# Optimization experiments

Hardware: AMD Instinct MI355X
Metric: run time of the kernel (lower is better)

Reference implementation:

```python
import jax, jax.numpy as jnp
import numpy as np

B, S, H, NH = 4, 1024, 2048, 16
HD = H // NH  # 128


def _rotate_half(x):
    x1, x2 = jnp.split(x, 2, axis=-1)
    return jnp.concatenate([-x2, x1], axis=-1)


def setup_inputs() -> dict:
    key = jax.random.key(0)
    ks = jax.random.split(key, 8)
    hidden_states = jax.random.normal(ks[0], (B, S, H), dtype=jnp.float32)
    k_in = jax.random.normal(ks[1], (B * NH, HD, S), dtype=jnp.float32)  # [B*nh, hd, K]
    v_in = jax.random.normal(ks[2], (B, NH, S, HD), dtype=jnp.float32)   # [B, nh, K, hd]
    # causal additive mask [B, 1, Q, K]
    i = jnp.arange(S)[:, None]
    j = jnp.arange(S)[None, :]
    mask = jnp.where(j <= i, 0.0, -1e9).astype(jnp.float32)
    attention_mask = jnp.broadcast_to(mask, (B, 1, S, S))
    # RoPE tables [S, hd]
    inv_freq = 1.0 / (10000.0 ** (jnp.arange(0, HD, 2, dtype=jnp.float32) / HD))
    freqs = jnp.arange(S, dtype=jnp.float32)[:, None] * inv_freq[None, :]  # [S, hd/2]
    emb = jnp.concatenate([freqs, freqs], axis=-1)  # [S, hd]
    rope_cos = jnp.cos(emb)
    rope_sin = jnp.sin(emb)
    std = 0.02
    wq = jax.random.normal(ks[3], (H, H), dtype=jnp.float32) * std
    bq = jnp.zeros((H,), dtype=jnp.float32)
    wo = jax.random.normal(ks[4], (H, H), dtype=jnp.float32) * (std / np.sqrt(2 * 24))
    bo = jnp.zeros((H,), dtype=jnp.float32)
    return {"hidden_states": hidden_states, "key": k_in, "value": v_in,
            "attention_mask": attention_mask, "rope_cos": rope_cos,
            "rope_sin": rope_sin, "wq": wq, "bq": bq, "wo": wo, "bo": bo}


def reference(hidden_states, key, value, attention_mask, rope_cos, rope_sin, wq, bq, wo, bo):
    dtype = hidden_states.dtype
    scale = 1.0 / np.sqrt(HD)
    # q projection -> [B, nh, Q, hd]
    q = hidden_states @ wq.T + bq
    q = q.reshape(B, S, NH, HD).transpose(0, 2, 1, 3)
    # RoPE on query only
    cos = rope_cos[None, None, :, :]
    sin = rope_sin[None, None, :, :]
    q = q * cos + _rotate_half(q) * sin
    # scores: key is [B*nh, hd, K]
    k = key.reshape(B, NH, HD, S)
    scores = jnp.einsum('bhqd,bhdk->bhqk', q, k) * scale + attention_mask
    probs = jax.nn.softmax(scores.astype(jnp.float32), axis=-1).astype(dtype)
    # attention output -> [B, Q, H]
    out = jnp.einsum('bhqk,bhkd->bqhd', probs, value).reshape(B, S, H)
    out = out @ wo.T + bo
    return out
```

## Files before the change

kernel.cpp:

```cpp
#include <hip/hip_runtime.h>
#include <cstdint>


typedef unsigned short u16;
typedef __bf16 bf16x8 __attribute__((ext_vector_type(8)));
typedef float  f32x4  __attribute__((ext_vector_type(4)));
typedef float  f32x16 __attribute__((ext_vector_type(16)));
typedef uint32_t u32x4 __attribute__((ext_vector_type(4)));

__device__ __forceinline__ u16 f2bf(float f) {
  uint32_t u = __builtin_bit_cast(uint32_t, f);
  u += 0x7fffu + ((u >> 16) & 1u);
  return (u16)(u >> 16);
}
__device__ __forceinline__ float bf2f(u16 h) {
  uint32_t u = ((uint32_t)h) << 16;
  return __builtin_bit_cast(float, u);
}
__device__ __forceinline__ uint32_t cvtpk(float lo, float hi) {
  uint32_t r;
  asm("v_cvt_pk_bf16_f32 %0, %1, %2" : "=v"(r) : "v"(lo), "v"(hi));
  return r;
}
__device__ __forceinline__ void gld16(const void* g, void* l) {
  __builtin_amdgcn_global_load_lds(
      (const __attribute__((address_space(1))) void*)g,
      (__attribute__((address_space(3))) void*)l, 16, 0, 0);
}

__global__ __launch_bounds__(256) void cvt_kernel(const float* __restrict__ in,
                                                  u16* __restrict__ out, int n4) {
  int i = blockIdx.x * 256 + threadIdx.x;
  if (i < n4) {
    float4 v = ((const float4*)in)[i];
    ushort4 o;
    o.x = f2bf(v.x); o.y = f2bf(v.y); o.z = f2bf(v.z); o.w = f2bf(v.w);
    ((ushort4*)out)[i] = o;
  }
}

__global__ __launch_bounds__(256) void transpose_cvt(const float* __restrict__ in,
                                                     u16* __restrict__ out, int R, int C) {
  __shared__ float tile[32][33];
  const int bh = blockIdx.x;
  const int nct = C >> 5;
  const int rt = blockIdx.y / nct, ct = blockIdx.y % nct;
  const float* src = in + (size_t)bh * R * C;
  u16* dst = out + (size_t)bh * R * C;
  const int r = threadIdx.x >> 3, c4 = (threadIdx.x & 7) * 4;
  float4 v = *(const float4*)(src + (size_t)(rt * 32 + r) * C + ct * 32 + c4);
  tile[r][c4 + 0] = v.x; tile[r][c4 + 1] = v.y;
  tile[r][c4 + 2] = v.z; tile[r][c4 + 3] = v.w;
  __syncthreads();
  ushort4 o;
  o.x = f2bf(tile[c4 + 0][r]); o.y = f2bf(tile[c4 + 1][r]);
  o.z = f2bf(tile[c4 + 2][r]); o.w = f2bf(tile[c4 + 3][r]);
  *(ushort4*)(dst + (size_t)(ct * 32 + r) * R + rt * 32 + c4) = o;
}

template<bool OUT_BF16>
__global__ __launch_bounds__(256, 2)
void gemm_bt(const u16* __restrict__ A, const u16* __restrict__ Bm,
             const float* __restrict__ bias, void* __restrict__ Cout,
             int M, int N, int K) {
  __shared__ __align__(16) u16 As[128 * 32];
  __shared__ __align__(16) u16 Bs[128 * 32];
  const int t = threadIdx.x, lane = t & 63, w = t >> 6;
  const int row0 = blockIdx.x * 128, col0 = blockIdx.y * 128;
  const int wr = (w >> 1) * 64, wc = (w & 1) * 64;
  const int fr = lane & 15, fg = lane >> 4, fk = fg * 8;
  const int srow = w * 32 + (lane >> 2), scol = (lane & 3) * 8;
  const u16* gA0 = A  + (size_t)(row0 + srow) * K + scol;
  const u16* gB0 = Bm + (size_t)(col0 + srow) * K + scol;
  u16* lA0 = As + (w * 32) * 32;
  u16* lA1 = As + (w * 32 + 16) * 32;
  u16* lB0 = Bs + (w * 32) * 32;
  u16* lB1 = Bs + (w * 32 + 16) * 32;
  f32x4 acc[4][4] = {};

  for (int k0 = 0; k0 < K; k0 += 32) {
    __syncthreads();
    gld16(gA0 + k0, lA0);
    gld16(gA0 + k0 + (size_t)16 * K, lA1);
    gld16(gB0 + k0, lB0);
    gld16(gB0 + k0 + (size_t)16 * K, lB1);
    __syncthreads();
    bf16x8 af[4], bq[4];
#pragma unroll
    for (int i = 0; i < 4; i++) af[i] = *(const bf16x8*)&As[(wr + i * 16 + fr) * 32 + fk];
#pragma unroll
    for (int i = 0; i < 4; i++) bq[i] = *(const bf16x8*)&Bs[(wc + i * 16 + fr) * 32 + fk];
#pragma unroll
    for (int mi = 0; mi < 4; mi++)
#pragma unroll
      for (int ni = 0; ni < 4; ni++)
        acc[mi][ni] = __builtin_amdgcn_mfma_f32_16x16x32_bf16(af[mi], bq[ni], acc[mi][ni], 0, 0, 0);
  }

#pragma unroll
  for (int mi = 0; mi < 4; mi++)
#pragma unroll
    for (int ni = 0; ni < 4; ni++) {
      int col = col0 + wc + ni * 16 + fr;
      float bv = bias[col];
#pragma unroll
      for (int i = 0; i < 4; i++) {
        int row = row0 + wr + mi * 16 + fg * 4 + i;
        float v = acc[mi][ni][i] + bv;
        if constexpr (OUT_BF16) ((u16*)Cout)[(size_t)row * N + col] = f2bf(v);
        else                    ((float*)Cout)[(size_t)row * N + col] = v;
      }
    }
}

__global__ __launch_bounds__(256, 2)
void gemm_rope(const u16* __restrict__ A, const u16* __restrict__ Bm,
               const float* __restrict__ bias, const float* __restrict__ cosb,
               const float* __restrict__ sinb, u16* __restrict__ qout) {
  __shared__ __align__(16) u16 As[128 * 32];
  __shared__ __align__(16) u16 Bs[128 * 32];
  const int K = 2048;
  const float SL2E = 0.12751743f;
  const int t = threadIdx.x, lane = t & 63, w = t >> 6;
  const int row0 = blockIdx.x * 128, h = blockIdx.y;
  const int wr = (w >> 1) * 64, g = w & 1;
  const int fr = lane & 15, fg = lane >> 4, fk = fg * 8;
  const int srow = w * 32 + (lane >> 2), scol = (lane & 3) * 8;
  const u16* gA0 = A  + (size_t)(row0 + srow) * K + scol;
  const u16* gB0 = Bm + (size_t)(h * 128 + srow) * K + scol;
  u16* lA0 = As + (w * 32) * 32;
  u16* lA1 = As + (w * 32 + 16) * 32;
  u16* lB0 = Bs + (w * 32) * 32;
  u16* lB1 = Bs + (w * 32 + 16) * 32;
  f32x4 acc[4][4] = {};
  const int colr[4] = {g * 32 + fr, g * 32 + 16 + fr,
                       g * 32 + 64 + fr, g * 32 + 80 + fr};

  for (int k0 = 0; k0 < K; k0 += 32) {
    __syncthreads();
    gld16(gA0 + k0, lA0);
    gld16(gA0 + k0 + (size_t)16 * K, lA1);
    gld16(gB0 + k0, lB0);
    gld16(gB0 + k0 + (size_t)16 * K, lB1);
    __syncthreads();
    bf16x8 af[4], bq[4];
#pragma unroll
    for (int i = 0; i < 4; i++) af[i] = *(const bf16x8*)&As[(wr + i * 16 + fr) * 32 + fk];
#pragma unroll
    for (int ni = 0; ni < 4; ni++) bq[ni] = *(const bf16x8*)&Bs[colr[ni] * 32 + fk];
#pragma unroll
    for (int mi = 0; mi < 4; mi++)
#pragma unroll
      for (int ni = 0; ni < 4; ni++)
        acc[mi][ni] = __builtin_amdgcn_mfma_f32_16x16x32_bf16(af[mi], bq[ni], acc[mi][ni], 0, 0, 0);
  }

  float bv[4];
#pragma unroll
  for (int ni = 0; ni < 4; ni++) bv[ni] = bias[h * 128 + colr[ni]];
#pragma unroll
  for (int mi = 0; mi < 4; mi++)
#pragma unroll
    for (int i = 0; i < 4; i++) {
      int row = row0 + wr + mi * 16 + fg * 4 + i;
      int s = row & 1023, bb = row >> 10;
      size_t obase = (((size_t)(bb * 16 + h)) * 1024 + s) * 128;
#pragma unroll
      for (int dp = 0; dp < 2; dp++) {
        int d = g * 32 + dp * 16 + fr;
        float c  = cosb[s * 128 + d] * SL2E;
        float sn = sinb[s * 128 + d] * SL2E;
        float qlo = acc[mi][dp][i] + bv[dp];
        float qhi = acc[mi][dp + 2][i] + bv[dp + 2];
        qout[obase + d]      = f2bf(qlo * c - qhi * sn);
        qout[obase + d + 64] = f2bf(qhi * c + qlo * sn);
      }
    }
}

__global__ __launch_bounds__(256, 1)
void attn_kernel(const u16* __restrict__ qbf, const u16* __restrict__ kTb,
                 const u16* __restrict__ vTb, u16* __restrict__ aout) {
  __shared__ __align__(16) u16 Kb[2][64 * 128];
  __shared__ __align__(16) u16 Vb[2][128 * 64];
  const int t = threadIdx.x, lane = t & 63, w = t >> 6;
  const int x = blockIdx.x;
  const int qt = 7 - (x >> 6);
  const int bh = x & 63;
  const int b = bh >> 4, h = bh & 15;
  const int q31 = lane & 31, hi = lane >> 5, kx7 = q31 & 7;
  const u16* kbase = kTb + (size_t)bh * 131072;
  const u16* vbase = vTb + (size_t)bh * 131072;

  const int kRow = t >> 4;
  const int kCb  = (t & 15) ^ (kRow & 7);
  const int vRow = t >> 3;
  const int vCb  = (t & 7) ^ (vRow & 7);

  const int rw0 = qt * 128 + w * 32;
  const int rowg = rw0 + q31;
  const int last = 2 * qt + 1;
  const int wlast = 2 * qt + (w >> 1);

  bf16x8 qf[8];
#pragma unroll
  for (int ds = 0; ds < 8; ds++)
    qf[ds] = *(const bf16x8*)&qbf[((size_t)bh * 1024 + rowg) * 128 + ds * 16 + hi * 8];

  f32x16 acc[4] = {};
  float m = -3e38f, l = 0.f;

  auto STAGE = [&](int kt, int buf) {
    const u16* ks = kbase + (size_t)(kt * 64 + kRow) * 128 + kCb * 8;
    const u16* vs = vbase + (size_t)vRow * 1024 + kt * 64 + vCb * 8;
    u16* kl = &Kb[buf][t * 8];
    u16* vl = &Vb[buf][t * 8];
#pragma unroll
    for (int p = 0; p < 4; p++) {
      gld16(ks + (size_t)p * 16 * 128, kl + p * 2048);
      gld16(vs + (size_t)p * 32 * 1024, vl + p * 2048);
    }
  };

  STAGE(0, 0);
  __syncthreads();
  for (int kt = 0; kt <= last; kt++) {
    const int cur = kt & 1;
    if (kt < last) STAGE(kt + 1, cur ^ 1);
    if (kt <= wlast) {
      f32x16 sa0 = {}, sa1 = {};
      __builtin_amdgcn_s_setprio(1);
#pragma unroll
      for (int ds = 0; ds < 8; ds++) {
        bf16x8 k0 = *(const bf16x8*)&Kb[cur][q31 * 128 + (((2 * ds + hi) ^ kx7) * 8)];
        bf16x8 k1 = *(const bf16x8*)&Kb[cur][(q31 + 32) * 128 + (((2 * ds + hi) ^ kx7) * 8)];
        sa0 = __builtin_amdgcn_mfma_f32_32x32x16_bf16(k0, qf[ds], sa0, 0, 0, 0);
        sa1 = __builtin_amdgcn_mfma_f32_32x32x16_bf16(k1, qf[ds], sa1, 0, 0, 0);
      }
      __builtin_amdgcn_s_setprio(0);

      if (kt == wlast) {
#pragma unroll
        for (int rr = 0; rr < 16; rr++) {
          int cr = (rr & 3) + 8 * (rr >> 2) + 4 * hi;
          if (kt * 64 + cr > rowg)      sa0[rr] = -1e9f;
          if (kt * 64 + 32 + cr > rowg) sa1[rr] = -1e9f;
        }
      }
      float t0 = fmaxf(fmaxf(sa0[0], sa0[1]), sa0[2]);
      float t1 = fmaxf(fmaxf(sa0[3], sa0[4]), sa0[5]);
      float t2 = fmaxf(fmaxf(sa0[6], sa0[7]), sa0[8]);
      float t3 = fmaxf(fmaxf(sa0[9], sa0[10]), sa0[11]);
      float t4 = fmaxf(fmaxf(sa0[12], sa0[13]), sa0[14]);
      float u0 = fmaxf(fmaxf(sa1[0], sa1[1]), sa1[2]);
      float u1 = fmaxf(fmaxf(sa1[3], sa1[4]), sa1[5]);
      float u2 = fmaxf(fmaxf(sa1[6], sa1[7]), sa1[8]);
      float u3 = fmaxf(fmaxf(sa1[9], sa1[10]), sa1[11]);
      float u4 = fmaxf(fmaxf(sa1[12], sa1[13]), sa1[14]);
      float mx = fmaxf(fmaxf(fmaxf(fmaxf(t0, t1), fmaxf(t2, t3)),
                             fmaxf(fmaxf(t4, sa0[15]), fmaxf(u0, u1))),
                       fmaxf(fmaxf(u2, u3), fmaxf(u4, sa1[15])));
      mx = fmaxf(mx, __shfl_xor(mx, 32));
      if (!__all(mx - m <= 11.5f)) {
        float mn = fmaxf(m, mx);
        float corr = __builtin_amdgcn_exp2f(m - mn);
        m = mn; l *= corr;
#pragma unroll
        for (int nd = 0; nd < 4; nd++)
#pragma unroll
          for (int rr = 0; rr < 16; rr++) acc[nd][rr] *= corr;
      }
#pragma unroll
      for (int rr = 0; rr < 16; rr++) {
        sa0[rr] = __builtin_amdgcn_exp2f(sa0[rr] - m);
        sa1[rr] = __builtin_amdgcn_exp2f(sa1[rr] - m);
      }
      {
        float s0 = (sa0[0] + sa0[1]) + (sa0[2] + sa0[3]);
        float s1 = (sa0[4] + sa0[5]) + (sa0[6] + sa0[7]);
        float s2 = (sa0[8] + sa0[9]) + (sa0[10] + sa0[11]);
        float s3 = (sa0[12] + sa0[13]) + (sa0[14] + sa0[15]);
        float s4 = (sa1[0] + sa1[1]) + (sa1[2] + sa1[3]);
        float s5 = (sa1[4] + sa1[5]) + (sa1[6] + sa1[7]);
        float s6 = (sa1[8] + sa1[9]) + (sa1[10] + sa1[11]);
        float s7 = (sa1[12] + sa1[13]) + (sa1[14] + sa1[15]);
        float sum = ((s0 + s1) + (s2 + s3)) + ((s4 + s5) + (s6 + s7));
        sum += __shfl_xor(sum, 32);
        l += sum;
      }

      __builtin_amdgcn_s_setprio(1);
      uint32_t wA = cvtpk(sa0[0], sa0[1]),   wB = cvtpk(sa0[2], sa0[3]);
      uint32_t wC = cvtpk(sa0[4], sa0[5]),   wD = cvtpk(sa0[6], sa0[7]);
      uint32_t wE = cvtpk(sa0[8], sa0[9]),   wF = cvtpk(sa0[10], sa0[11]);
      uint32_t wG = cvtpk(sa0[12], sa0[13]), wH = cvtpk(sa0[14], sa0[15]);
      uint32_t wI = cvtpk(sa1[0], sa1[1]),   wJ = cvtpk(sa1[2], sa1[3]);
      uint32_t wK = cvtpk(sa1[4], sa1[5]),   wL = cvtpk(sa1[6], sa1[7]);
      uint32_t wM = cvtpk(sa1[8], sa1[9]),   wN = cvtpk(sa1[10], sa1[11]);
      uint32_t wO = cvtpk(sa1[12], sa1[13]), wP = cvtpk(sa1[14], sa1[15]);
      uint32_t xA = __shfl_xor(wA, 32), xB = __shfl_xor(wB, 32);
      uint32_t xC = __shfl_xor(wC, 32), xD = __shfl_xor(wD, 32);
      uint32_t xE = __shfl_xor(wE, 32), xF = __shfl_xor(wF, 32);
      uint32_t xG = __shfl_xor(wG, 32), xH = __shfl_xor(wH, 32);
      uint32_t xI = __shfl_xor(wI, 32), xJ = __shfl_xor(wJ, 32);
      uint32_t xK = __shfl_xor(wK, 32), xL = __shfl_xor(wL, 32);
      uint32_t xM = __shfl_xor(wM, 32), xN = __shfl_xor(wN, 32);
      uint32_t xO = __shfl_xor(wO, 32), xP = __shfl_xor(wP, 32);
#pragma unroll
      for (int ks = 0; ks < 4; ks++) {
        u32x4 aw;
        if (ks == 0) {
          aw.x = hi ? xC : wA;  aw.y = hi ? xD : wB;
          aw.z = hi ? wC : xA;  aw.w = hi ? wD : xB;
        } else if (ks == 1) {
          aw.x = hi ? xG : wE;  aw.y = hi ? xH : wF;
          aw.z = hi ? wG : xE;  aw.w = hi ? wH : xF;
        } else if (ks == 2) {
          aw.x = hi ? xK : wI;  aw.y = hi ? xL : wJ;
          aw.z = hi ? wK : xI;  aw.w = hi ? wL : xJ;
        } else {
          aw.x = hi ? xO : wM;  aw.y = hi ? xP : wN;
          aw.z = hi ? wO : xM;  aw.w = hi ? wP : xN;
        }
        bf16x8 af = __builtin_bit_cast(bf16x8, aw);
#pragma unroll
        for (int nd = 0; nd < 4; nd++) {
          bf16x8 vf = *(const bf16x8*)&Vb[cur][(nd * 32 + q31) * 64 + (((2 * ks + hi) ^ kx7) * 8)];
          acc[nd] = __builtin_amdgcn_mfma_f32_32x32x16_bf16(af, vf, acc[nd], 0, 0, 0);
        }
      }
      __builtin_amdgcn_s_setprio(0);
    }
    __syncthreads();
  }

  float linv = 1.f / l;
#pragma unroll
  for (int rr = 0; rr < 16; rr++) {
    int cr = (rr & 3) + 8 * (rr >> 2) + 4 * hi;
    float li = __shfl(linv, cr);
    int sg = rw0 + cr;
    size_t obase = (((size_t)b * 1024 + sg) * 16 + h) * 128 + q31;
#pragma unroll
    for (int nd = 0; nd < 4; nd++)
      aout[obase + nd * 32] = f2bf(acc[nd][rr] * li);
  }
}

extern "C" void kernel_launch(void* const* d_in, const int* in_sizes, int n_in,
                              void* d_out, int out_size, void* d_ws, size_t ws_size,
                              hipStream_t stream) {
  const float* hs  = (const float*)d_in[0];
  const float* key = (const float*)d_in[1];
  const float* val = (const float*)d_in[2];
  const float* rc  = (const float*)d_in[4];
  const float* rs  = (const float*)d_in[5];
  const float* wq  = (const float*)d_in[6];
  const float* bq  = (const float*)d_in[7];
  const float* wo  = (const float*)d_in[8];
  const float* bo  = (const float*)d_in[9];
  float* out = (float*)d_out;

  char* ws = (char*)d_ws;
  u16* hs_bf = (u16*)(ws);
  u16* wq_bf = (u16*)(ws + 16777216);
  u16* wo_bf = (u16*)(ws + 25165824);
  u16* q_bf  = (u16*)(ws + 33554432);
  u16* kT    = (u16*)(ws + 50331648);
  u16* vT    = (u16*)(ws + 67108864);
  u16* attn_bf = hs_bf;

  cvt_kernel<<<8192, 256, 0, stream>>>(hs, hs_bf, 8388608 / 4);
  cvt_kernel<<<4096, 256, 0, stream>>>(wq, wq_bf, 4194304 / 4);
  cvt_kernel<<<4096, 256, 0, stream>>>(wo, wo_bf, 4194304 / 4);

  transpose_cvt<<<dim3(64, 128), 256, 0, stream>>>(key, kT, 128, 1024);
  transpose_cvt<<<dim3(64, 128), 256, 0, stream>>>(val, vT, 1024, 128);

  gemm_rope<<<dim3(32, 16), 256, 0, stream>>>(hs_bf, wq_bf, bq, rc, rs, q_bf);
  attn_kernel<<<512, 256, 0, stream>>>(q_bf, kT, vT, attn_bf);
  gemm_bt<false><<<dim3(32, 16), 256, 0, stream>>>(attn_bf, wo_bf, bo, out, 4096, 2048, 2048);
}
```

Before: 182.3 us.

## Replace both GEMMs with 256x128-tile triple-buffered pipelined GEMM kernel

Merges the Q-projection+RoPE GEMM and output-projection GEMM into one templated kernel with 256x128 tiles, 512 threads, BK=64, a three-stage LDS ring fed by global_load_lds with vmcnt-based waits, XOR-swizzled LDS layout, and split prefetch interleaved with MFMA halves under raised wave priority. The aim is to hide global-load latency and reduce LDS bank conflicts and barrier overhead compared with the single-buffered 128x128 BK=32 loop. The grid drops to 256 blocks at one block per CU, which may underfill the 256-CU device's latency hiding, and the large LDS footprint limits occupancy.

Measured after the change: 160.6 us. 11.9% less time.

```diff
diff --git a/kernel.cpp b/kernel.cpp
--- a/kernel.cpp
+++ b/kernel.cpp
@@ -12,10 +12,6 @@
   uint32_t u = __builtin_bit_cast(uint32_t, f);
   u += 0x7fffu + ((u >> 16) & 1u);
   return (u16)(u >> 16);
-}
-__device__ __forceinline__ float bf2f(u16 h) {
-  uint32_t u = ((uint32_t)h) << 16;
-  return __builtin_bit_cast(float, u);
 }
 __device__ __forceinline__ uint32_t cvtpk(float lo, float hi) {
   uint32_t r;
@@ -58,124 +54,142 @@
   *(ushort4*)(dst + (size_t)(ct * 32 + r) * R + rt * 32 + c4) = o;
 }
 
-template<bool OUT_BF16>
-__global__ __launch_bounds__(256, 2)
-void gemm_bt(const u16* __restrict__ A, const u16* __restrict__ Bm,
-             const float* __restrict__ bias, void* __restrict__ Cout,
-             int M, int N, int K) {
-  __shared__ __align__(16) u16 As[128 * 32];
-  __shared__ __align__(16) u16 Bs[128 * 32];
+template<int MODE>
+__global__ __launch_bounds__(512, 1)
+void gemm256(const u16* __restrict__ A, const u16* __restrict__ Bm,
+             const float* __restrict__ bias, const float* __restrict__ cosb,
+             const float* __restrict__ sinb, void* __restrict__ Cout) {
+  constexpr int K = 2048, N = 2048, NT = 32;
+  __shared__ __align__(16) u16 LA[3][256 * 64];
+  __shared__ __align__(16) u16 LB[3][128 * 64];
   const int t = threadIdx.x, lane = t & 63, w = t >> 6;
-  const int row0 = blockIdx.x * 128, col0 = blockIdx.y * 128;
-  const int wr = (w >> 1) * 64, wc = (w & 1) * 64;
-  const int fr = lane & 15, fg = lane >> 4, fk = fg * 8;
-  const int srow = w * 32 + (lane >> 2), scol = (lane & 3) * 8;
-  const u16* gA0 = A  + (size_t)(row0 + srow) * K + scol;
-  const u16* gB0 = Bm + (size_t)(col0 + srow) * K + scol;
-  u16* lA0 = As + (w * 32) * 32;
-  u16* lA1 = As + (w * 32 + 16) * 32;
-  u16* lB0 = Bs + (w * 32) * 32;
-  u16* lB1 = Bs + (w * 32 + 16) * 32;
+  const int row0 = blockIdx.x * 256, col0 = blockIdx.y * 128;
+  const int wr = (w >> 1) * 64;
+  const int g = w & 1;
+  const int fr = lane & 15, fg = lane >> 4, fx = fr & 7;
+  const int sb8 = ((t & 7) ^ ((t >> 3) & 7)) * 8;
+  const u16* gA = A  + (size_t)(row0 + (t >> 3)) * K + sb8;
+  const u16* gB = Bm + (size_t)(col0 + (t >> 3)) * K + sb8;
+  const int lo8 = t * 8;
+
+  int brow[4];
+  if constexpr (MODE == 1) {
+    brow[0] = g * 32 + fr;      brow[1] = g * 32 + 16 + fr;
+    brow[2] = g * 32 + 64 + fr; brow[3] = g * 32 + 80 + fr;
+  } else {
+    brow[0] = g * 64 + fr;      brow[1] = g * 64 + 16 + fr;
+    brow[2] = g * 64 + 32 + fr; brow[3] = g * 64 + 48 + fr;
+  }
+
   f32x4 acc[4][4] = {};
 
-  for (int k0 = 0; k0 < K; k0 += 32) {
-    __syncthreads();
-    gld16(gA0 + k0, lA0);
-    gld16(gA0 + k0 + (size_t)16 * K, lA1);
-    gld16(gB0 + k0, lB0);
-    gld16(gB0 + k0 + (size_t)16 * K, lB1);
-    __syncthreads();
-    bf16x8 af[4], bq[4];
-#pragma unroll
-    for (int i = 0; i < 4; i++) af[i] = *(const bf16x8*)&As[(wr + i * 16 + fr) * 32 + fk];
-#pragma unroll
-    for (int i = 0; i < 4; i++) bq[i] = *(const bf16x8*)&Bs[(wc + i * 16 + fr) * 32 + fk];
+  auto SA0 = [&](int kt, int buf) {
+    const int k0 = kt * 64;
+    gld16(gA + k0,                    &LA[buf][lo8]);
+    gld16(gA + k0 + (size_t)64 * K,   &LA[buf][4096 + lo8]);
+    gld16(gB + k0,                    &LB[buf][lo8]);
+  };
+  auto SA1 = [&](int kt, int buf) {
+    const int k0 = kt * 64;
+    gld16(gA + k0 + (size_t)128 * K,  &LA[buf][8192 + lo8]);
+    gld16(gA + k0 + (size_t)192 * K,  &LA[buf][12288 + lo8]);
+    gld16(gB + k0 + (size_t)64 * K,   &LB[buf][4096 + lo8]);
+  };
+
+  SA0(0, 0); SA1(0, 0);
+  SA0(1, 1); SA1(1, 1);
+
+  int cb = 0;
+  for (int kt = 0; kt < NT; ++kt) {
+    const int sbuf = cb >= 1 ? cb - 1 : cb + 2;
+    if (kt < NT - 1) asm volatile("s_waitcnt vmcnt(6)" ::: "memory");
+    else             asm volatile("s_waitcnt vmcnt(0)" ::: "memory");
+    __builtin_amdgcn_s_barrier();
+    asm volatile("" ::: "memory");
+
+    bf16x8 af[4][2], bq0[2][2];
 #pragma unroll
     for (int mi = 0; mi < 4; mi++)
 #pragma unroll
-      for (int ni = 0; ni < 4; ni++)
-        acc[mi][ni] = __builtin_amdgcn_mfma_f32_16x16x32_bf16(af[mi], bq[ni], acc[mi][ni], 0, 0, 0);
-  }
-
-#pragma unroll
-  for (int mi = 0; mi < 4; mi++)
-#pragma unroll
-    for (int ni = 0; ni < 4; ni++) {
-      int col = col0 + wc + ni * 16 + fr;
-      float bv = bias[col];
+      for (int ks = 0; ks < 2; ks++)
+        af[mi][ks] = *(const bf16x8*)&LA[cb][(wr + mi * 16 + fr) * 64 + ((ks * 4 + fg) ^ fx) * 8];
+#pragma unroll
+    for (int ni = 0; ni < 2; ni++)
+#pragma unroll
+      for (int ks = 0; ks < 2; ks++)
+        bq0[ni][ks] = *(const bf16x8*)&LB[cb][brow[ni] * 64 + ((ks * 4 + fg) ^ fx) * 8];
+    if (kt + 2 < NT) SA0(kt + 2, sbuf);
+    __builtin_amdgcn_s_setprio(1);
+#pragma unroll
+    for (int ks = 0; ks < 2; ks++)
+#pragma unroll
+      for (int mi = 0; mi < 4; mi++)
+#pragma unroll
+        for (int ni = 0; ni < 2; ni++)
+          acc[mi][ni] = __builtin_amdgcn_mfma_f32_16x16x32_bf16(af[mi][ks], bq0[ni][ks], acc[mi][ni], 0, 0, 0);
+    __builtin_amdgcn_s_setprio(0);
+    __builtin_amdgcn_s_barrier();
+    asm volatile("" ::: "memory");
+
+    bf16x8 bq1[2][2];
+#pragma unroll
+    for (int ni = 0; ni < 2; ni++)
+#pragma unroll
+      for (int ks = 0; ks < 2; ks++)
+        bq1[ni][ks] = *(const bf16x8*)&LB[cb][brow[ni + 2] * 64 + ((ks * 4 + fg) ^ fx) * 8];
+    if (kt + 2 < NT) SA1(kt + 2, sbuf);
+    __builtin_amdgcn_s_setprio(1);
+#pragma unroll
+    for (int ks = 0; ks < 2; ks++)
+#pragma unroll
+      for (int mi = 0; mi < 4; mi++)
+#pragma unroll
+        for (int ni = 0; ni < 2; ni++)
+          acc[mi][ni + 2] = __builtin_amdgcn_mfma_f32_16x16x32_bf16(af[mi][ks], bq1[ni][ks], acc[mi][ni + 2], 0, 0, 0);
+    __builtin_amdgcn_s_setprio(0);
+
+    cb = cb == 2 ? 0 : cb + 1;
+  }
+
+  if constexpr (MODE == 0) {
+#pragma unroll
+    for (int mi = 0; mi < 4; mi++)
+#pragma unroll
+      for (int ni = 0; ni < 4; ni++) {
+        int col = col0 + brow[ni];
+        float bv = bias[col];
+#pragma unroll
+        for (int i = 0; i < 4; i++) {
+          int row = row0 + wr + mi * 16 + fg * 4 + i;
+          ((float*)Cout)[(size_t)row * N + col] = acc[mi][ni][i] + bv;
+        }
+      }
+  } else {
+    const int h = blockIdx.y;
+    const float SL2E = 0.12751743f;
+    float bv[4];
+#pragma unroll
+    for (int ni = 0; ni < 4; ni++) bv[ni] = bias[h * 128 + brow[ni]];
+    u16* qout = (u16*)Cout;
+#pragma unroll
+    for (int mi = 0; mi < 4; mi++)
 #pragma unroll
       for (int i = 0; i < 4; i++) {
         int row = row0 + wr + mi * 16 + fg * 4 + i;
-        float v = acc[mi][ni][i] + bv;
-        if constexpr (OUT_BF16) ((u16*)Cout)[(size_t)row * N + col] = f2bf(v);
-        else                    ((float*)Cout)[(size_t)row * N + col] = v;
-      }
-    }
-}
-
-__global__ __launch_bounds__(256, 2)
-void gemm_rope(const u16* __restrict__ A, const u16* __restrict__ Bm,
-               const float* __restrict__ bias, const float* __restrict__ cosb,
-               const float* __restrict__ sinb, u16* __restrict__ qout) {
-  __shared__ __align__(16) u16 As[128 * 32];
-  __shared__ __align__(16) u16 Bs[128 * 32];
-  const int K = 2048;
-  const float SL2E = 0.12751743f;
-  const int t = threadIdx.x, lane = t & 63, w = t >> 6;
-  const int row0 = blockIdx.x * 128, h = blockIdx.y;
-  const int wr = (w >> 1) * 64, g = w & 1;
-  const int fr = lane & 15, fg = lane >> 4, fk = fg * 8;
-  const int srow = w * 32 + (lane >> 2), scol = (lane & 3) * 8;
-  const u16* gA0 = A  + (size_t)(row0 + srow) * K + scol;
-  const u16* gB0 = Bm + (size_t)(h * 128 + srow) * K + scol;
-  u16* lA0 = As + (w * 32) * 32;
-  u16* lA1 = As + (w * 32 + 16) * 32;
-  u16* lB0 = Bs + (w * 32) * 32;
-  u16* lB1 = Bs + (w * 32 + 16) * 32;
-  f32x4 acc[4][4] = {};
-  const int colr[4] = {g * 32 + fr, g * 32 + 16 + fr,
-                       g * 32 + 64 + fr, g * 32 + 80 + fr};
-
-  for (int k0 = 0; k0 < K; k0 += 32) {
-    __syncthreads();
-    gld16(gA0 + k0, lA0);
-    gld16(gA0 + k0 + (size_t)16 * K, lA1);
-    gld16(gB0 + k0, lB0);
-    gld16(gB0 + k0 + (size_t)16 * K, lB1);
-    __syncthreads();
-    bf16x8 af[4], bq[4];
-#pragma unroll
-    for (int i = 0; i < 4; i++) af[i] = *(const bf16x8*)&As[(wr + i * 16 + fr) * 32 + fk];
-#pragma unroll
-    for (int ni = 0; ni < 4; ni++) bq[ni] = *(const bf16x8*)&Bs[colr[ni] * 32 + fk];
-#pragma unroll
-    for (int mi = 0; mi < 4; mi++)
-#pragma unroll
-      for (int ni = 0; ni < 4; ni++)
-        acc[mi][ni] = __builtin_amdgcn_mfma_f32_16x16x32_bf16(af[mi], bq[ni], acc[mi][ni], 0, 0, 0);
-  }
-
-  float bv[4];
-#pragma unroll
-  for (int ni = 0; ni < 4; ni++) bv[ni] = bias[h * 128 + colr[ni]];
-#pragma unroll
-  for (int mi = 0; mi < 4; mi++)
-#pragma unroll
-    for (int i = 0; i < 4; i++) {
-      int row = row0 + wr + mi * 16 + fg * 4 + i;
-      int s = row & 1023, bb = row >> 10;
-      size_t obase = (((size_t)(bb * 16 + h)) * 1024 + s) * 128;
-#pragma unroll
-      for (int dp = 0; dp < 2; dp++) {
-        int d = g * 32 + dp * 16 + fr;
-        float c  = cosb[s * 128 + d] * SL2E;
-        float sn = sinb[s * 128 + d] * SL2E;
-        float qlo = acc[mi][dp][i] + bv[dp];
-        float qhi = acc[mi][dp + 2][i] + bv[dp + 2];
-        qout[obase + d]      = f2bf(qlo * c - qhi * sn);
-        qout[obase + d + 64] = f2bf(qhi * c + qlo * sn);
-      }
-    }
+        int s = row & 1023, bb = row >> 10;
+        size_t obase = (((size_t)(bb * 16 + h)) * 1024 + s) * 128;
+#pragma unroll
+        for (int dp = 0; dp < 2; dp++) {
+          int d = g * 32 + dp * 16 + fr;
+          float c  = cosb[s * 128 + d] * SL2E;
+          float sn = sinb[s * 128 + d] * SL2E;
+          float qlo = acc[mi][dp][i] + bv[dp];
+          float qhi = acc[mi][dp + 2][i] + bv[dp + 2];
+          qout[obase + d]      = f2bf(qlo * c - qhi * sn);
+          qout[obase + d + 64] = f2bf(qhi * c + qlo * sn);
+        }
+      }
+  }
 }
 
 __global__ __launch_bounds__(256, 1)
@@ -377,7 +391,7 @@
   transpose_cvt<<<dim3(64, 128), 256, 0, stream>>>(key, kT, 128, 1024);
   transpose_cvt<<<dim3(64, 128), 256, 0, stream>>>(val, vT, 1024, 128);
 
-  gemm_rope<<<dim3(32, 16), 256, 0, stream>>>(hs_bf, wq_bf, bq, rc, rs, q_bf);
+  gemm256<1><<<dim3(16, 16), 512, 0, stream>>>(hs_bf, wq_bf, bq, rc, rs, q_bf);
   attn_kernel<<<512, 256, 0, stream>>>(q_bf, kT, vT, attn_bf);
-  gemm_bt<false><<<dim3(32, 16), 256, 0, stream>>>(attn_bf, wo_bf, bo, out, 4096, 2048, 2048);
-}
+  gemm256<0><<<dim3(16, 16), 512, 0, stream>>>(attn_bf, wo_bf, bo, nullptr, nullptr, out);
+}
```
